# Kernel tuning notes

Hardware: AMD Instinct MI355X
Metric: run time of the kernel (lower is better)

## Reference

```python
import jax, jax.numpy as jnp
import numpy as np

N_NODES = 50000
N_EDGES = 800000
IN_F = 256
OUT_F = 64
HEADS = 4
NEG_SLOPE = 0.2


def setup_inputs() -> dict:
    key = jax.random.key(0)
    ks = jax.random.split(key, 6)
    x = jax.random.normal(ks[0], (N_NODES, IN_F), dtype=jnp.float32)
    edge_index = jax.random.randint(ks[1], (2, N_EDGES), 0, N_NODES, dtype=jnp.int32)
    edge_weight = jax.random.uniform(ks[2], (N_EDGES,), dtype=jnp.float32)
    # Xavier-uniform-ish scale for params
    gain = float(np.sqrt(2.0 / (1.0 + NEG_SLOPE ** 2)))
    w_bound = gain * np.sqrt(6.0 / (IN_F + OUT_F))
    a_bound = gain * np.sqrt(6.0 / (OUT_F + 1))
    W = jax.random.uniform(ks[3], (HEADS, IN_F, OUT_F), minval=-w_bound, maxval=w_bound, dtype=jnp.float32)
    a_src = jax.random.uniform(ks[4], (HEADS, OUT_F, 1), minval=-a_bound, maxval=a_bound, dtype=jnp.float32)
    a_dst = jax.random.uniform(ks[5], (HEADS, OUT_F, 1), minval=-a_bound, maxval=a_bound, dtype=jnp.float32)
    return {"x": x, "edge_index": edge_index, "edge_weight": edge_weight,
            "W": W, "a_src": a_src, "a_dst": a_dst}


def reference(x, edge_index, edge_weight, W, a_src, a_dst):
    num_nodes = x.shape[0]
    # Per-head linear projection: [H, N, out]
    h = jnp.einsum('ni,hio->hno', x, W)
    # Per-node attention logits, [H, N]
    attn_src = jnp.einsum('hno,hod->hn', h, a_src)
    attn_dst = jnp.einsum('hno,hod->hn', h, a_dst)
    src_idx, dst_idx = edge_index[0], edge_index[1]
    # Per-edge scores [H, E]
    e = attn_src[:, src_idx] + attn_dst[:, dst_idx]
    e = jnp.where(e >= 0, e, NEG_SLOPE * e)  # leaky_relu
    e = e * edge_weight[None, :]
    # Global-max-stabilized exp (matches original: single global max)
    e_exp = jnp.exp(e - jnp.max(e))
    # Segment-softmax denominator per dst node, [H, N]
    denom = jax.ops.segment_sum(e_exp.T, dst_idx, num_segments=num_nodes).T
    alpha = e_exp / (denom[:, dst_idx] + 1e-10)  # [H, E]
    # Weighted messages and scatter-add aggregation
    msg = h[:, src_idx] * alpha[..., None]  # [H, E, out]
    out = jax.vmap(lambda m: jax.ops.segment_sum(m, dst_idx, num_segments=num_nodes))(msg)  # [H, N, out]
    # concat=True: [N, H*out]
    return jnp.transpose(out, (1, 0, 2)).reshape(num_nodes, HEADS * OUT_F)
```

## Files before the change

### kernel.cpp

```cpp
#include <hip/hip_runtime.h>

#define N_NODES 50000
#define N_EDGES 800000
#define IN_F 256
#define OUT_F 64
#define HEADS 4
#define HF 256
#define NEG_SLOPE 0.2f
#define CAP 48

typedef __bf16 bf16x8 __attribute__((ext_vector_type(8)));
typedef float f32x4 __attribute__((ext_vector_type(4)));

__device__ __forceinline__ unsigned encf(float f) {
  unsigned u = __float_as_uint(f);
  return (u & 0x80000000u) ? ~u : (u | 0x80000000u);
}
__device__ __forceinline__ float decf(unsigned k) {
  unsigned u = (k & 0x80000000u) ? (k & 0x7FFFFFFFu) : ~k;
  return __uint_as_float(u);
}
__device__ __forceinline__ unsigned short f2bf(float f) {
  unsigned u = __float_as_uint(f);
  u += 0x7FFFu + ((u >> 16) & 1u);
  return (unsigned short)(u >> 16);
}
__device__ __forceinline__ float bflo(unsigned u) { return __uint_as_float(u << 16); }
__device__ __forceinline__ float bfhi(unsigned u) { return __uint_as_float(u & 0xFFFF0000u); }

__device__ __forceinline__ float emax4(float4 a, float4 b, float w) {
  float v0 = a.x + b.x, v1 = a.y + b.y, v2 = a.z + b.z, v3 = a.w + b.w;
  v0 = v0 >= 0.f ? v0 : NEG_SLOPE * v0;
  v1 = v1 >= 0.f ? v1 : NEG_SLOPE * v1;
  v2 = v2 >= 0.f ? v2 : NEG_SLOPE * v2;
  v3 = v3 >= 0.f ? v3 : NEG_SLOPE * v3;
  return fmaxf(fmaxf(v0 * w, v1 * w), fmaxf(v2 * w, v3 * w));
}

__global__ __launch_bounds__(256) void k_init_wa(const float* __restrict__ W,
                                                 const float* __restrict__ a_src,
                                                 const float* __restrict__ a_dst,
                                                 float* __restrict__ wa_src,
                                                 float* __restrict__ wa_dst) {
  int hd = blockIdx.x;
  int k = threadIdx.x;
  const float* wrow = W + ((size_t)hd * IN_F + k) * OUT_F;
  const float* asv = a_src + hd * OUT_F;
  const float* adv = a_dst + hd * OUT_F;
  float ss = 0.f, sd = 0.f;
#pragma unroll
  for (int o = 0; o < OUT_F; o += 4) {
    float4 w4 = *(const float4*)(wrow + o);
    float4 s4 = *(const float4*)(asv + o);
    float4 d4 = *(const float4*)(adv + o);
    ss += w4.x * s4.x + w4.y * s4.y + w4.z * s4.z + w4.w * s4.w;
    sd += w4.x * d4.x + w4.y * d4.y + w4.z * d4.z + w4.w * d4.w;
  }
  wa_src[hd * IN_F + k] = ss;
  wa_dst[hd * IN_F + k] = sd;
}

__global__ __launch_bounds__(256) void k_prep(const float* __restrict__ x,
                                              const float* __restrict__ W,
                                              const int* __restrict__ src,
                                              const int* __restrict__ dst,
                                              const float* __restrict__ ew,
                                              const float* __restrict__ wa_src,
                                              const float* __restrict__ wa_dst,
                                              unsigned short* __restrict__ xb,
                                              unsigned short* __restrict__ wb,
                                              int* __restrict__ deg,
                                              int2* __restrict__ rec,
                                              float* __restrict__ as,
                                              float* __restrict__ ad) {
  int tid = blockIdx.x * 256 + threadIdx.x;
  const float* px = x + (size_t)tid * 8;
  float4 v0 = *(const float4*)px;
  float4 v1 = *(const float4*)(px + 4);
  {
    uint4 o;
    o.x = (unsigned)f2bf(v0.x) | ((unsigned)f2bf(v0.y) << 16);
    o.y = (unsigned)f2bf(v0.z) | ((unsigned)f2bf(v0.w) << 16);
    o.z = (unsigned)f2bf(v1.x) | ((unsigned)f2bf(v1.y) << 16);
    o.w = (unsigned)f2bf(v1.z) | ((unsigned)f2bf(v1.w) << 16);
    *(uint4*)(xb + (size_t)tid * 8) = o;
  }
  if (tid < N_EDGES) {
    int d = dst[tid];
    int s = src[tid];
    float w = ew[tid];
    int r = atomicAdd(deg + d, 1);
    if (r < CAP) rec[d * CAP + r] = make_int2(s, __float_as_int(w));
  }
  if (tid < 65536) {
    int j = tid & 7, l = (tid >> 3) & 63, kt = (tid >> 9) & 7;
    int w = (tid >> 12) & 3, hd = (tid >> 14) & 3;
    int k = kt * 32 + (l >> 4) * 8 + j;
    int o = w * 16 + (l & 15);
    wb[tid] = f2bf(W[((size_t)hd * IN_F + k) * OUT_F + o]);
  }
  {
    int k0 = (tid & 31) * 8;
    float ps[4], pd[4];
#pragma unroll
    for (int hd = 0; hd < 4; hd++) {
      float4 s0 = *(const float4*)(wa_src + hd * IN_F + k0);
      float4 s1 = *(const float4*)(wa_src + hd * IN_F + k0 + 4);
      float4 d0 = *(const float4*)(wa_dst + hd * IN_F + k0);
      float4 d1 = *(const float4*)(wa_dst + hd * IN_F + k0 + 4);
      ps[hd] = v0.x * s0.x + v0.y * s0.y + v0.z * s0.z + v0.w * s0.w
             + v1.x * s1.x + v1.y * s1.y + v1.z * s1.z + v1.w * s1.w;
      pd[hd] = v0.x * d0.x + v0.y * d0.y + v0.z * d0.z + v0.w * d0.w
             + v1.x * d1.x + v1.y * d1.y + v1.z * d1.z + v1.w * d1.w;
    }
#pragma unroll
    for (int off = 16; off > 0; off >>= 1) {
#pragma unroll
      for (int hd = 0; hd < 4; hd++) {
        ps[hd] += __shfl_down(ps[hd], off, 32);
        pd[hd] += __shfl_down(pd[hd], off, 32);
      }
    }
    if ((tid & 31) == 0) {
      int m = tid >> 5;
      *(float4*)(as + (size_t)m * 4) = make_float4(ps[0], ps[1], ps[2], ps[3]);
      *(float4*)(ad + (size_t)m * 4) = make_float4(pd[0], pd[1], pd[2], pd[3]);
    }
  }
}

__global__ __launch_bounds__(256) void k_gemm_max(
    const unsigned short* __restrict__ xb, const unsigned short* __restrict__ wb,
    unsigned short* __restrict__ hb,
    const int* __restrict__ src, const int* __restrict__ dst,
    const float* __restrict__ ew, const float* __restrict__ as,
    const float* __restrict__ ad, unsigned* __restrict__ gmax) {
  const int t = threadIdx.x;

  if (blockIdx.x & 1) {
    int t4 = (blockIdx.x >> 1) * 256 + t;
    int e0 = t4 * 4;
    bool ok = e0 < N_EDGES;
    int4 s4 = ok ? *(const int4*)(src + e0) : make_int4(0, 0, 0, 0);
    int4 d4 = ok ? *(const int4*)(dst + e0) : make_int4(0, 0, 0, 0);
    float4 w4 = ok ? *(const float4*)(ew + e0) : make_float4(0.f, 0.f, 0.f, 0.f);
    float4 A0, B0, A1, B1, A2, B2, A3, B3;
    if (ok) {
      A0 = *(const float4*)(as + (size_t)s4.x * 4);
      B0 = *(const float4*)(ad + (size_t)d4.x * 4);
      A1 = *(const float4*)(as + (size_t)s4.y * 4);
      B1 = *(const float4*)(ad + (size_t)d4.y * 4);
      A2 = *(const float4*)(as + (size_t)s4.z * 4);
      B2 = *(const float4*)(ad + (size_t)d4.z * 4);
      A3 = *(const float4*)(as + (size_t)s4.w * 4);
      B3 = *(const float4*)(ad + (size_t)d4.w * 4);
    } else {
      A0 = B0 = A1 = B1 = A2 = B2 = A3 = B3 = make_float4(0.f, 0.f, 0.f, 0.f);
    }
    float m = -3.4e38f;
    if (ok) {
      m = fmaxf(fmaxf(emax4(A0, B0, w4.x), emax4(A1, B1, w4.y)),
                fmaxf(emax4(A2, B2, w4.z), emax4(A3, B3, w4.w)));
    }
#pragma unroll
    for (int off = 32; off > 0; off >>= 1) m = fmaxf(m, __shfl_down(m, off));
    __shared__ float red[4];
    int wave = t >> 6, lane = t & 63;
    if (lane == 0) red[wave] = m;
    __syncthreads();
    if (t == 0) {
      float mm = fmaxf(fmaxf(red[0], red[1]), fmaxf(red[2], red[3]));
      atomicMax(gmax, encf(mm));
    }
    return;
  }

  const int hd = t >> 6, l = t & 63;
  const int quad = l >> 4, col = l & 15;
  const int blk = blockIdx.x >> 1;
  f32x4 acc[4][4];
#pragma unroll
  for (int ms = 0; ms < 4; ms++)
#pragma unroll
    for (int nt = 0; nt < 4; nt++) acc[ms][nt] = (f32x4){0.f, 0.f, 0.f, 0.f};

  const unsigned short* ab[4];
#pragma unroll
  for (int ms = 0; ms < 4; ms++) {
    int mt = blk * 4 + ms;
    if (mt > 3124) mt = 3124;
    ab[ms] = xb + (size_t)(mt * 16 + col) * IN_F + quad * 8;
  }
  const unsigned short* wbase = wb + (size_t)hd * 16384 + l * 8;

  for (int kt = 0; kt < 8; kt++) {
    union { uint4 u; bf16x8 v; } b[4], a[4];
#pragma unroll
    for (int nt = 0; nt < 4; nt++)
      b[nt].u = *(const uint4*)(wbase + (nt * 8 + kt) * 512);
#pragma unroll
    for (int ms = 0; ms < 4; ms++)
      a[ms].u = *(const uint4*)(ab[ms] + kt * 32);
#pragma unroll
    for (int ms = 0; ms < 4; ms++)
#pragma unroll
      for (int nt = 0; nt < 4; nt++)
        acc[ms][nt] = __builtin_amdgcn_mfma_f32_16x16x32_bf16(a[ms].v, b[nt].v, acc[ms][nt], 0, 0, 0);
  }

#pragma unroll
  for (int ms = 0; ms < 4; ms++) {
    int mbase = blk * 64 + ms * 16 + quad * 4;
#pragma unroll
    for (int r = 0; r < 4; r++) {
      int m = mbase + r;
      if (m < N_NODES) {
#pragma unroll
        for (int nt = 0; nt < 4; nt++)
          hb[(size_t)m * HF + hd * OUT_F + nt * 16 + col] = f2bf(acc[ms][nt][r]);
      }
    }
  }
}

__global__ __launch_bounds__(256) void k_agg(const int* __restrict__ deg,
                                             const int2* __restrict__ rec,
                                             const float* __restrict__ as,
                                             const float* __restrict__ ad,
                                             const unsigned* __restrict__ gmax,
                                             const unsigned short* __restrict__ hb,
                                             float* __restrict__ out) {
  __shared__ float sal[4][4][68];
  const int t = threadIdx.x;
  const int wv = t >> 6, lane = t & 63;
  const int half = lane >> 5, li = lane & 31;
  const int hd8 = li >> 3;
  const int d = blockIdx.x * 4 + wv;
  const int rs = d * CAP;
  const int dg = min(deg[d], CAP);
  const float gm = decf(*gmax);
  const float4 adv = *(const float4*)(ad + (size_t)d * 4);
  float ax = 0.f, ay = 0.f, az = 0.f, aw = 0.f;
  float bx = 0.f, by = 0.f, bz = 0.f, bw = 0.f;
  float den = 0.f;

  for (int j0 = 0; j0 < dg; j0 += 64) {
    const int nj = min(64, dg - j0);
    int se = 0;
    float we = 0.f;
    if (lane < nj) {
      int2 r = rec[rs + j0 + lane];
      se = r.x;
      we = __int_as_float(r.y);
    }
    {
      float4 a4 = *(const float4*)(as + (size_t)se * 4);
      float v0 = a4.x + adv.x;
      float v1 = a4.y + adv.y;
      float v2 = a4.z + adv.z;
      float v3 = a4.w + adv.w;
      v0 = v0 >= 0.f ? v0 : NEG_SLOPE * v0;
      v1 = v1 >= 0.f ? v1 : NEG_SLOPE * v1;
      v2 = v2 >= 0.f ? v2 : NEG_SLOPE * v2;
      v3 = v3 >= 0.f ? v3 : NEG_SLOPE * v3;
      bool okj = lane < nj;
      sal[wv][0][lane] = okj ? __expf(v0 * we - gm) : 0.f;
      sal[wv][1][lane] = okj ? __expf(v1 * we - gm) : 0.f;
      sal[wv][2][lane] = okj ? __expf(v2 * we - gm) : 0.f;
      sal[wv][3][lane] = okj ? __expf(v3 * we - gm) : 0.f;
    }
    asm volatile("s_waitcnt lgkmcnt(0)" ::: "memory");
    const float* salh = sal[wv][hd8];

    int j = 0;
    for (; j + 7 < nj; j += 8) {
      int sj0 = __shfl(se, j + half);
      int sj1 = __shfl(se, j + 2 + half);
      int sj2 = __shfl(se, j + 4 + half);
      int sj3 = __shfl(se, j + 6 + half);
      uint4 q0 = *(const uint4*)(hb + (size_t)sj0 * HF + li * 8);
      uint4 q1 = *(const uint4*)(hb + (size_t)sj1 * HF + li * 8);
      uint4 q2 = *(const uint4*)(hb + (size_t)sj2 * HF + li * 8);
      uint4 q3 = *(const uint4*)(hb + (size_t)sj3 * HF + li * 8);
      float a0 = salh[j + half];
      float a1 = salh[j + 2 + half];
      float a2 = salh[j + 4 + half];
      float a3 = salh[j + 6 + half];
      den += (a0 + a1) + (a2 + a3);
      ax += a0 * bflo(q0.x) + a1 * bflo(q1.x) + a2 * bflo(q2.x) + a3 * bflo(q3.x);
      ay += a0 * bfhi(q0.x) + a1 * bfhi(q1.x) + a2 * bfhi(q2.x) + a3 * bfhi(q3.x);
      az += a0 * bflo(q0.y) + a1 * bflo(q1.y) + a2 * bflo(q2.y) + a3 * bflo(q3.y);
      aw += a0 * bfhi(q0.y) + a1 * bfhi(q1.y) + a2 * bfhi(q2.y) + a3 * bfhi(q3.y);
      bx += a0 * bflo(q0.z) + a1 * bflo(q1.z) + a2 * bflo(q2.z) + a3 * bflo(q3.z);
      by += a0 * bfhi(q0.z) + a1 * bfhi(q1.z) + a2 * bfhi(q2.z) + a3 * bfhi(q3.z);
      bz += a0 * bflo(q0.w) + a1 * bflo(q1.w) + a2 * bflo(q2.w) + a3 * bflo(q3.w);
      bw += a0 * bfhi(q0.w) + a1 * bfhi(q1.w) + a2 * bfhi(q2.w) + a3 * bfhi(q3.w);
    }
    for (; j < nj; j += 2) {
      int sj0 = __shfl(se, min(j + half, nj - 1));
      float a0 = (j + half < nj) ? salh[j + half] : 0.f;
      uint4 q0 = *(const uint4*)(hb + (size_t)sj0 * HF + li * 8);
      den += a0;
      ax += a0 * bflo(q0.x);
      ay += a0 * bfhi(q0.x);
      az += a0 * bflo(q0.y);
      aw += a0 * bfhi(q0.y);
      bx += a0 * bflo(q0.z);
      by += a0 * bfhi(q0.z);
      bz += a0 * bflo(q0.w);
      bw += a0 * bfhi(q0.w);
    }
  }

  ax += __shfl_xor(ax, 32); ay += __shfl_xor(ay, 32);
  az += __shfl_xor(az, 32); aw += __shfl_xor(aw, 32);
  bx += __shfl_xor(bx, 32); by += __shfl_xor(by, 32);
  bz += __shfl_xor(bz, 32); bw += __shfl_xor(bw, 32);
  den += __shfl_xor(den, 32);
  float inv = 1.f / (den + 1e-10f);
  float4 r;
  if (half == 0) r = make_float4(ax * inv, ay * inv, az * inv, aw * inv);
  else           r = make_float4(bx * inv, by * inv, bz * inv, bw * inv);
  *(float4*)(out + (size_t)d * HF + li * 8 + half * 4) = r;
}

extern "C" void kernel_launch(void* const* d_in, const int* in_sizes, int n_in,
                              void* d_out, int out_size, void* d_ws, size_t ws_size,
                              hipStream_t stream) {
  const float* x     = (const float*)d_in[0];
  const int*   ei    = (const int*)d_in[1];
  const float* ew    = (const float*)d_in[2];
  const float* W     = (const float*)d_in[3];
  const float* a_src = (const float*)d_in[4];
  const float* a_dst = (const float*)d_in[5];
  float* out = (float*)d_out;

  unsigned short* hb = (unsigned short*)d_ws;
  unsigned short* xb = hb + (size_t)N_NODES * HF;
  unsigned short* wbp = xb + (size_t)N_NODES * IN_F;
  float* as = (float*)(wbp + 65536);
  float* ad = as + (size_t)HEADS * N_NODES;
  float* wa_src = ad + (size_t)HEADS * N_NODES;
  float* wa_dst = wa_src + HEADS * IN_F;
  int* deg       = (int*)(wa_dst + HEADS * IN_F);
  unsigned* gmax = (unsigned*)(deg + N_NODES);
  int2* rec      = (int2*)(gmax + 1);

  const int* srcp = ei;
  const int* dstp = ei + N_EDGES;

  hipMemsetAsync(deg, 0, (size_t)(N_NODES + 1) * sizeof(int), stream);
  k_init_wa<<<4, 256, 0, stream>>>(W, a_src, a_dst, wa_src, wa_dst);
  k_prep<<<6250, 256, 0, stream>>>(x, W, srcp, dstp, ew, wa_src, wa_dst,
                                   xb, wbp, deg, rec, as, ad);
  k_gemm_max<<<1564, 256, 0, stream>>>(xb, wbp, hb, srcp, dstp, ew, as, ad, gmax);
  k_agg<<<N_NODES / 4, 256, 0, stream>>>(deg, rec, as, ad, gmax, hb, out);
}
```

Measured before the change: 267.8 us.

## Split edge bucketing: rank via atomics in prep, scatter records in gemm kernel

The memset and the weight-attention precompute are merged into one init kernel, which removes a separate memset call. Edge bucketing is split in two. The prep kernel now only does the degree atomicAdd and stores each edge's rank. The scattered record writes move into the max-reduction half of the GEMM kernel, which already loads src, dst and weight, so the scatter can overlap with GEMM blocks. The cost is an extra rank array of N_EDGES ints that is written and then read back.

```diff
diff --git a/kernel.cpp b/kernel.cpp
--- a/kernel.cpp
+++ b/kernel.cpp
@@ -37,12 +37,20 @@
   return fmaxf(fmaxf(v0 * w, v1 * w), fmaxf(v2 * w, v3 * w));
 }
 
-__global__ __launch_bounds__(256) void k_init_wa(const float* __restrict__ W,
-                                                 const float* __restrict__ a_src,
-                                                 const float* __restrict__ a_dst,
-                                                 float* __restrict__ wa_src,
-                                                 float* __restrict__ wa_dst) {
-  int hd = blockIdx.x;
+__global__ __launch_bounds__(256) void k_init(const float* __restrict__ W,
+                                              const float* __restrict__ a_src,
+                                              const float* __restrict__ a_dst,
+                                              int* __restrict__ deg,
+                                              unsigned* __restrict__ gmax,
+                                              float* __restrict__ wa_src,
+                                              float* __restrict__ wa_dst) {
+  if (blockIdx.x < 196) {
+    int i = blockIdx.x * 256 + threadIdx.x;
+    if (i < N_NODES) deg[i] = 0;
+    if (i == 0) *gmax = 0u;
+    return;
+  }
+  int hd = blockIdx.x - 196;
   int k = threadIdx.x;
   const float* wrow = W + ((size_t)hd * IN_F + k) * OUT_F;
   const float* asv = a_src + hd * OUT_F;
@@ -62,15 +70,13 @@
 
 __global__ __launch_bounds__(256) void k_prep(const float* __restrict__ x,
                                               const float* __restrict__ W,
-                                              const int* __restrict__ src,
                                               const int* __restrict__ dst,
-                                              const float* __restrict__ ew,
                                               const float* __restrict__ wa_src,
                                               const float* __restrict__ wa_dst,
                                               unsigned short* __restrict__ xb,
                                               unsigned short* __restrict__ wb,
                                               int* __restrict__ deg,
-                                              int2* __restrict__ rec,
+                                              int* __restrict__ rank,
                                               float* __restrict__ as,
                                               float* __restrict__ ad) {
   int tid = blockIdx.x * 256 + threadIdx.x;
@@ -85,13 +91,7 @@
     o.w = (unsigned)f2bf(v1.z) | ((unsigned)f2bf(v1.w) << 16);
     *(uint4*)(xb + (size_t)tid * 8) = o;
   }
-  if (tid < N_EDGES) {
-    int d = dst[tid];
-    int s = src[tid];
-    float w = ew[tid];
-    int r = atomicAdd(deg + d, 1);
-    if (r < CAP) rec[d * CAP + r] = make_int2(s, __float_as_int(w));
-  }
+  if (tid < N_EDGES) rank[tid] = atomicAdd(deg + dst[tid], 1);
   if (tid < 65536) {
     int j = tid & 7, l = (tid >> 3) & 63, kt = (tid >> 9) & 7;
     int w = (tid >> 12) & 3, hd = (tid >> 14) & 3;
@@ -129,12 +129,13 @@
   }
 }
 
-__global__ __launch_bounds__(256) void k_gemm_max(
+__global__ __launch_bounds__(256) void k_gemm_scatter(
     const unsigned short* __restrict__ xb, const unsigned short* __restrict__ wb,
     unsigned short* __restrict__ hb,
     const int* __restrict__ src, const int* __restrict__ dst,
-    const float* __restrict__ ew, const float* __restrict__ as,
-    const float* __restrict__ ad, unsigned* __restrict__ gmax) {
+    const float* __restrict__ ew, const int* __restrict__ rank,
+    const float* __restrict__ as, const float* __restrict__ ad,
+    int2* __restrict__ rec, unsigned* __restrict__ gmax) {
   const int t = threadIdx.x;
 
   if (blockIdx.x & 1) {
@@ -144,6 +145,8 @@
     int4 s4 = ok ? *(const int4*)(src + e0) : make_int4(0, 0, 0, 0);
     int4 d4 = ok ? *(const int4*)(dst + e0) : make_int4(0, 0, 0, 0);
     float4 w4 = ok ? *(const float4*)(ew + e0) : make_float4(0.f, 0.f, 0.f, 0.f);
+    int4 r4 = ok ? *(const int4*)(rank + e0) : make_int4(0, 0, 0, 0);
+
     float4 A0, B0, A1, B1, A2, B2, A3, B3;
     if (ok) {
       A0 = *(const float4*)(as + (size_t)s4.x * 4);
@@ -156,6 +159,12 @@
       B3 = *(const float4*)(ad + (size_t)d4.w * 4);
     } else {
       A0 = B0 = A1 = B1 = A2 = B2 = A3 = B3 = make_float4(0.f, 0.f, 0.f, 0.f);
+    }
+    if (ok) {
+      if (r4.x < CAP) rec[d4.x * CAP + r4.x] = make_int2(s4.x, __float_as_int(w4.x));
+      if (r4.y < CAP) rec[d4.y * CAP + r4.y] = make_int2(s4.y, __float_as_int(w4.y));
+      if (r4.z < CAP) rec[d4.z * CAP + r4.z] = make_int2(s4.z, __float_as_int(w4.z));
+      if (r4.w < CAP) rec[d4.w * CAP + r4.w] = make_int2(s4.w, __float_as_int(w4.w));
     }
     float m = -3.4e38f;
     if (ok) {
@@ -344,15 +353,15 @@
   float* wa_dst = wa_src + HEADS * IN_F;
   int* deg       = (int*)(wa_dst + HEADS * IN_F);
   unsigned* gmax = (unsigned*)(deg + N_NODES);
-  int2* rec      = (int2*)(gmax + 1);
+  int* rank      = (int*)(gmax + 1);
+  int2* rec      = (int2*)(rank + N_EDGES);
 
   const int* srcp = ei;
   const int* dstp = ei + N_EDGES;
 
-  hipMemsetAsync(deg, 0, (size_t)(N_NODES + 1) * sizeof(int), stream);
-  k_init_wa<<<4, 256, 0, stream>>>(W, a_src, a_dst, wa_src, wa_dst);
-  k_prep<<<6250, 256, 0, stream>>>(x, W, srcp, dstp, ew, wa_src, wa_dst,
-                                   xb, wbp, deg, rec, as, ad);
-  k_gemm_max<<<1564, 256, 0, stream>>>(xb, wbp, hb, srcp, dstp, ew, as, ad, gmax);
+  k_init<<<200, 256, 0, stream>>>(W, a_src, a_dst, deg, gmax, wa_src, wa_dst);
+  k_prep<<<6250, 256, 0, stream>>>(x, W, dstp, wa_src, wa_dst, xb, wbp, deg, rank, as, ad);
+  k_gemm_scatter<<<1564, 256, 0, stream>>>(xb, wbp, hb, srcp, dstp, ew, rank,
+                                           as, ad, rec, gmax);
   k_agg<<<N_NODES / 4, 256, 0, stream>>>(deg, rec, as, ad, gmax, hb, out);
 }
```

After: 250.5 us. 1.07x faster.
